# Optimization experiments

Hardware: AMD Instinct MI355X
Metric: run time of the kernel (lower is better)

The kernel has to match this reference:

```python
import jax, jax.numpy as jnp
import numpy as np

B, S, D = 4, 2048, 1024
H = 16
HD = D // H  # head dim = 64


def setup_inputs() -> dict:
    key = jax.random.key(0)
    ks = jax.random.split(key, 9)
    sc = 1.0 / np.sqrt(D)
    return {
        "x": jax.random.normal(ks[0], (B, S, D), jnp.float32),
        "Wq_w": jax.random.normal(ks[1], (D, D), jnp.float32) * sc,
        "Wq_b": jax.random.normal(ks[2], (D,), jnp.float32) * 0.01,
        "Wk_w": jax.random.normal(ks[3], (D, D), jnp.float32) * sc,
        "Wk_b": jax.random.normal(ks[4], (D,), jnp.float32) * 0.01,
        "Wv_w": jax.random.normal(ks[5], (D, D), jnp.float32) * sc,
        "Wv_b": jax.random.normal(ks[6], (D,), jnp.float32) * 0.01,
        "Wo_w": jax.random.normal(ks[7], (D, D), jnp.float32) * sc,
        "Wo_b": jax.random.normal(ks[8], (D,), jnp.float32) * 0.01,
    }


def reference(x, Wq_w, Wq_b, Wk_w, Wk_b, Wv_w, Wv_b, Wo_w, Wo_b):
    b, s, _ = x.shape
    # QKV projections (weights stored [in, out])
    q = x @ Wq_w + Wq_b
    k = x @ Wk_w + Wk_b
    v = x @ Wv_w + Wv_b
    # [b, s, D] -> [b, H, s, hd]
    q = q.reshape(b, s, H, HD).transpose(0, 2, 1, 3)
    k = k.reshape(b, s, H, HD).transpose(0, 2, 1, 3)
    v = v.reshape(b, s, H, HD).transpose(0, 2, 1, 3)
    # naive attention: full [b, H, s, s] scores, scale by head_dim**0.5
    scores = jnp.einsum("bhqd,bhkd->bhqk", q, k) / jnp.sqrt(jnp.float32(HD))
    # faithful to torch: tril(scores)==0 -> -inf (causal mask via tril of values)
    filt = jnp.tril(scores)
    scores = jnp.where(filt == 0, jnp.float32(-jnp.inf), scores)
    probs = jax.nn.softmax(scores, axis=-1)
    attn = jnp.einsum("bhqk,bhkd->bhqd", probs, v)
    # [b, H, s, hd] -> [b, s, D]
    attn = attn.transpose(0, 2, 1, 3).reshape(b, s, D)
    return attn @ Wo_w + Wo_b
```

## Files before the change

### kernel.cpp

```cpp
#include <hip/hip_runtime.h>
#include <hip/hip_bf16.h>


#define B_  4
#define S_  2048
#define D_  1024
#define H_  16
#define HD_ 64
#define M_  (B_*S_)
#define NT_ (S_/64)

typedef unsigned short u16;
typedef __attribute__((ext_vector_type(8))) short bf16x8;
typedef __attribute__((ext_vector_type(4))) float f32x4;
typedef __attribute__((ext_vector_type(8))) unsigned short ush8;
typedef __attribute__((ext_vector_type(4))) unsigned short ush4;

static __device__ __forceinline__ u16 f2b(float f) {
    unsigned int u = __float_as_uint(f);
    return (u16)((u + 0x7fffu + ((u >> 16) & 1u)) >> 16);
}

static __device__ __forceinline__ int cvt_pk_bf16(float a, float b) {
    int r;
    asm("v_cvt_pk_bf16_f32 %0, %1, %2" : "=v"(r) : "v"(a), "v"(b));
    return r;
}

#define EXP2(x) exp2f(x)

#define GLOAD_LDS16(g, l)                                                      \
    __builtin_amdgcn_global_load_lds(                                          \
        (const __attribute__((address_space(1))) void*)(g),                    \
        (__attribute__((address_space(3))) void*)(l), 16, 0, 0)

#define QSCALE 0.18033688f

__global__ __launch_bounds__(256)
void cast_f32_bf16(const float* __restrict__ in, u16* __restrict__ out, int n8)
{
    int i = blockIdx.x * blockDim.x + threadIdx.x;
    const int stride = gridDim.x * blockDim.x;
    for (; i < n8; i += stride) {
        const float4 a = ((const float4*)in)[i*2+0];
        const float4 b = ((const float4*)in)[i*2+1];
        ush8 o;
        o[0]=f2b(a.x); o[1]=f2b(a.y); o[2]=f2b(a.z); o[3]=f2b(a.w);
        o[4]=f2b(b.x); o[5]=f2b(b.y); o[6]=f2b(b.z); o[7]=f2b(b.w);
        ((ush8*)out)[i] = o;
    }
}

__global__ __launch_bounds__(256)
void transpose_cast(const float* __restrict__ W, u16* __restrict__ Wt)
{
    __shared__ u16 T[64*72];
    const int tid = threadIdx.x;
    const int k0 = blockIdx.x * 64, n0 = blockIdx.y * 64;
    #pragma unroll
    for (int it = 0; it < 4; ++it) {
        const int li = tid + it*256;
        const int kk = li >> 4;
        const int nc = (li & 15) * 4;
        const float4 w4 = *(const float4*)&W[(size_t)(k0+kk)*D_ + n0 + nc];
        T[(nc+0)*72 + kk] = f2b(w4.x);
        T[(nc+1)*72 + kk] = f2b(w4.y);
        T[(nc+2)*72 + kk] = f2b(w4.z);
        T[(nc+3)*72 + kk] = f2b(w4.w);
    }
    __syncthreads();
    #pragma unroll
    for (int it = 0; it < 2; ++it) {
        const int li = tid + it*256;
        const int nr = li >> 3;
        const int kc = (li & 7) * 8;
        const ush8 v = *(const ush8*)&T[nr*72 + kc];
        *(ush8*)&Wt[(size_t)(n0+nr)*D_ + k0 + kc] = v;
    }
}

__device__ __forceinline__ void gemm256_loop(
    const u16* __restrict__ Ag, size_t arow0,
    const u16* __restrict__ Bg, size_t brow0,
    u16* __restrict__ sh, f32x4 (&acc)[8][4])
{
    const int tid  = threadIdx.x;
    const int lane = tid & 63;
    const int wave = tid >> 6;
    const int wr = wave >> 2, wc = wave & 3;
    const int cl = lane & 15, g = lane >> 4;
    const int sw = cl & 7;
    u16* const Ab = sh;
    u16* const Bb = sh + 32768;

    const int srow   = lane >> 3;
    const int schunk = (lane & 7) ^ srow;

    auto stage_half = [&](const u16* gbase, size_t row0, int k0, u16* lbase) {
        #pragma unroll
        for (int i = 0; i < 2; ++i) {
            const int seg = wave*2 + i;
            const u16* src = gbase + (row0 + seg*8 + srow) * (size_t)D_
                                   + k0 + schunk*8;
            u16* dst = lbase + seg*512;
            GLOAD_LDS16(src, dst);
        }
    };

    stage_half(Ag, arow0,       0, Ab);
    stage_half(Ag, arow0 + 128, 0, Ab + 8192);
    stage_half(Bg, brow0,       0, Bb);
    stage_half(Bg, brow0 + 128, 0, Bb + 8192);
    __syncthreads();

    for (int t = 0; t < 16; ++t) {
        u16* const Ac = Ab + (t & 1) * 16384;
        u16* const Bc = Bb + (t & 1) * 16384;
        u16* const An = Ab + ((t + 1) & 1) * 16384;
        u16* const Bn = Bb + ((t + 1) & 1) * 16384;
        const int  kn   = (t + 1) * 64;
        const bool more = (t < 15);

        bf16x8 bfr[4][2];
        #pragma unroll
        for (int nf = 0; nf < 4; ++nf)
            #pragma unroll
            for (int ks = 0; ks < 2; ++ks)
                bfr[nf][ks] = *(const bf16x8*)
                    &Bc[(wc*64 + nf*16 + cl)*64 + (((ks*4 + g) ^ sw) * 8)];

        #pragma unroll
        for (int p = 0; p < 4; ++p) {
            bf16x8 af[2][2];
            #pragma unroll
            for (int e = 0; e < 2; ++e)
                #pragma unroll
                for (int ks = 0; ks < 2; ++ks)
                    af[e][ks] = *(const bf16x8*)
                        &Ac[(wr*128 + (p*2 + e)*16 + cl)*64
                            + (((ks*4 + g) ^ sw) * 8)];

            if (p == 0 && more) {
                stage_half(Ag, arow0,       kn, An);
                stage_half(Ag, arow0 + 128, kn, An + 8192);
            } else if (p == 1 && more) {
                stage_half(Bg, brow0,       kn, Bn);
                stage_half(Bg, brow0 + 128, kn, Bn + 8192);
            }

            __builtin_amdgcn_sched_barrier(0);
            __builtin_amdgcn_s_barrier();
            __builtin_amdgcn_sched_barrier(0);

            __builtin_amdgcn_s_setprio(1);
            #pragma unroll
            for (int e = 0; e < 2; ++e)
                #pragma unroll
                for (int ks = 0; ks < 2; ++ks)
                    #pragma unroll
                    for (int nf = 0; nf < 4; ++nf)
                        acc[p*2 + e][nf] = __builtin_amdgcn_mfma_f32_16x16x32_bf16(
                            af[e][ks], bfr[nf][ks], acc[p*2 + e][nf], 0, 0, 0);
            __builtin_amdgcn_s_setprio(0);

            if (p == 3) {
                asm volatile("s_waitcnt vmcnt(0)" ::: "memory");
            }
            __builtin_amdgcn_sched_barrier(0);
            __builtin_amdgcn_s_barrier();
            __builtin_amdgcn_sched_barrier(0);
        }
    }
    __syncthreads();
}

__global__ __launch_bounds__(512, 2)
void gemm_qkv256(const u16* __restrict__ A,
                 const u16* __restrict__ wq, const u16* __restrict__ wk,
                 const u16* __restrict__ wv,
                 const float* __restrict__ bq, const float* __restrict__ bk,
                 const float* __restrict__ bv,
                 u16* __restrict__ oq, u16* __restrict__ ok,
                 u16* __restrict__ ovt)
{
    __shared__ u16 sh[67584];

    const int tid  = threadIdx.x;
    const int lane = tid & 63;
    const int wave = tid >> 6;
    const int wr = wave >> 2, wc = wave & 3;
    const int cl = lane & 15, g = lane >> 4;
    const size_t bm = (size_t)blockIdx.x * 256;
    const int by   = blockIdx.y;
    const int sel  = by >> 2;
    const int bn2  = (by & 3) * 256;
    const u16* Bt = sel == 0 ? wq : sel == 1 ? wk : wv;
    const float* bias = sel == 0 ? bq : sel == 1 ? bk : bv;

    f32x4 acc[8][4];
    const f32x4 z4 = {0.f, 0.f, 0.f, 0.f};
    #pragma unroll
    for (int i = 0; i < 8; ++i)
        #pragma unroll
        for (int j = 0; j < 4; ++j) acc[i][j] = z4;

    gemm256_loop(A, bm, Bt, (size_t)bn2, sh, acc);

    if (sel == 2) {
        const int b  = (int)(bm >> 11);
        const int s0 = (int)(bm & (S_ - 1));
        #pragma unroll
        for (int nf = 0; nf < 4; ++nf) {
            const float bvv = bias[bn2 + wc*64 + nf*16 + cl];
            #pragma unroll
            for (int mf = 0; mf < 8; ++mf) {
                ush4 o4;
                #pragma unroll
                for (int r = 0; r < 4; ++r) o4[r] = f2b(acc[mf][nf][r] + bvv);
                *(ush4*)&sh[wc*16896 + (nf*16 + cl)*264 + wr*128 + mf*16 + g*4] = o4;
            }
        }
        __syncthreads();
        const int head = wave >> 1, shalf = wave & 1;
        const int hh = (bn2 >> 6) + head;
        #pragma unroll
        for (int it = 0; it < 16; ++it) {
            const int lin = it*64 + lane;
            const int d = lin >> 4, sc = lin & 15;
            const ush8 vv = *(const ush8*)&sh[head*16896 + d*264 + shalf*128 + sc*8];
            *(ush8*)&ovt[((size_t)((b*H_ + hh)*HD_ + d))*S_ + s0 + shalf*128 + sc*8] = vv;
        }
    } else {
        const float osc = sel == 0 ? QSCALE : 1.0f;
        u16* o = sel == 0 ? oq : ok;
        #pragma unroll
        for (int nf = 0; nf < 4; ++nf) {
            const int col = bn2 + wc*64 + nf*16 + cl;
            const float bvv = bias[col];
            const int h = col >> 6, d = col & (HD_ - 1);
            #pragma unroll
            for (int mf = 0; mf < 8; ++mf) {
                #pragma unroll
                for (int r = 0; r < 4; ++r) {
                    const size_t row = bm + wr*128 + mf*16 + g*4 + r;
                    const int bb = (int)(row >> 11), s = (int)(row & (S_ - 1));
                    o[((size_t)(bb*H_ + h)*S_ + s)*HD_ + d] =
                        f2b((acc[mf][nf][r] + bvv) * osc);
                }
            }
        }
    }
}

__global__ __launch_bounds__(512, 2)
void gemm_oproj256(const u16* __restrict__ A, const u16* __restrict__ Bt,
                   const float* __restrict__ bias, float* __restrict__ out)
{
    __shared__ u16 sh[65536];

    const int tid  = threadIdx.x;
    const int lane = tid & 63;
    const int wave = tid >> 6;
    const int wr = wave >> 2, wc = wave & 3;
    const int cl = lane & 15, g = lane >> 4;
    const size_t bm = (size_t)blockIdx.x * 256;
    const size_t bn = (size_t)blockIdx.y * 256;

    f32x4 acc[8][4];
    const f32x4 z4 = {0.f, 0.f, 0.f, 0.f};
    #pragma unroll
    for (int i = 0; i < 8; ++i)
        #pragma unroll
        for (int j = 0; j < 4; ++j) acc[i][j] = z4;

    gemm256_loop(A, bm, Bt, bn, sh, acc);

    #pragma unroll
    for (int nf = 0; nf < 4; ++nf) {
        const int col = (int)bn + wc*64 + nf*16 + cl;
        const float bvv = bias[col];
        #pragma unroll
        for (int mf = 0; mf < 8; ++mf) {
            #pragma unroll
            for (int r = 0; r < 4; ++r) {
                const size_t row = bm + wr*128 + mf*16 + g*4 + r;
                out[row*D_ + col] = acc[mf][nf][r] + bvv;
            }
        }
    }
}

__global__ __launch_bounds__(256, 4)
void attn_bf16(const u16* __restrict__ Q, const u16* __restrict__ K,
               const u16* __restrict__ Vt, u16* __restrict__ out)
{
    __shared__ u16 Ks[2][64*64];
    __shared__ u16 Vs[2][64*64];

    const int tid  = threadIdx.x;
    const int lane = tid & 63;
    const int wave = tid >> 6;
    const int cl = lane & 15;
    const int g  = lane >> 4;
    const int swz = cl & 7;
    const int pair = blockIdx.x, h = blockIdx.y, b = blockIdx.z;
    const size_t base  = ((size_t)(b*H_ + h)) * S_ * HD_;
    const size_t vbase = ((size_t)(b*H_ + h)) * HD_ * S_;

    int qt = pair;
    const int n0 = pair + 1;

    const int r0 = tid >> 3;
    const int c0 = tid & 7;

    bf16x8 qf[2];
    #pragma unroll
    for (int ks = 0; ks < 2; ++ks)
        qf[ks] = *(const bf16x8*)&Q[base +
            (size_t)(qt*64 + wave*16 + cl)*HD_ + ks*32 + g*8];

    ush8 kreg[2], vreg[2];
    #pragma unroll
    for (int p = 0; p < 2; ++p) {
        kreg[p] = *(const ush8*)&K [base  + (size_t)(r0 + p*32)*HD_ + c0*8];
        vreg[p] = *(const ush8*)&Vt[vbase + (size_t)(r0 + p*32)*S_  + c0*8];
    }

    const f32x4 z4 = {0.f, 0.f, 0.f, 0.f};
    f32x4 oac[4];
    float m_i = -3.0e38f, l_i = 0.f;
    #pragma unroll
    for (int nf = 0; nf < 4; ++nf) oac[nf] = z4;

    int cur = 0;
    for (int t = 0; t < NT_ + 1; ++t) {
        const int kt = (t >= n0) ? t - n0 : t;

        if (t == n0) {
            const float inv = 1.f / l_i;
            const int srow = qt*64 + wave*16 + cl;
            #pragma unroll
            for (int nf = 0; nf < 4; ++nf) {
                ush4 o4;
                #pragma unroll
                for (int r = 0; r < 4; ++r) o4[r] = f2b(oac[nf][r] * inv);
                *(ush4*)&out[(size_t)(b*S_ + srow)*D_ + h*HD_ + nf*16 + g*4] = o4;
            }
            qt = NT_ - 1 - pair;
            #pragma unroll
            for (int ks = 0; ks < 2; ++ks)
                qf[ks] = *(const bf16x8*)&Q[base +
                    (size_t)(qt*64 + wave*16 + cl)*HD_ + ks*32 + g*8];
            m_i = -3.0e38f; l_i = 0.f;
            #pragma unroll
            for (int nf = 0; nf < 4; ++nf) oac[nf] = z4;
        }

        #pragma unroll
        for (int p = 0; p < 2; ++p) {
            const int row = r0 + p*32;
            const int slot = (c0 ^ (row & 7)) * 8;
            *(ush8*)&Ks[cur][row*64 + slot] = kreg[p];
            *(ush8*)&Vs[cur][row*64 + slot] = vreg[p];
        }
        __syncthreads();

        if (t + 1 < NT_ + 1) {
            const int nkt = (t + 1 >= n0) ? t + 1 - n0 : t + 1;
            #pragma unroll
            for (int p = 0; p < 2; ++p) {
                kreg[p] = *(const ush8*)&K [base  +
                    (size_t)(nkt*64 + r0 + p*32)*HD_ + c0*8];
                vreg[p] = *(const ush8*)&Vt[vbase +
                    (size_t)(r0 + p*32)*S_ + nkt*64 + c0*8];
            }
        }

        f32x4 sac[4];
        #pragma unroll
        for (int nf = 0; nf < 4; ++nf) sac[nf] = z4;
        __builtin_amdgcn_s_setprio(1);
        #pragma unroll
        for (int ks = 0; ks < 2; ++ks) {
            const int slot = ((ks*4 + g) ^ swz) * 8;
            #pragma unroll
            for (int nf = 0; nf < 4; ++nf) {
                const bf16x8 kf =
                    *(const bf16x8*)&Ks[cur][(nf*16 + cl)*64 + slot];
                sac[nf] = __builtin_amdgcn_mfma_f32_16x16x32_bf16(
                    kf, qf[ks], sac[nf], 0, 0, 0);
            }
        }
        __builtin_amdgcn_s_setprio(0);

        if (kt == qt) {
            const int qloc = wave*16 + cl;
            #pragma unroll
            for (int nf = 0; nf < 4; ++nf)
                #pragma unroll
                for (int r = 0; r < 4; ++r)
                    if (nf*16 + g*4 + r > qloc) sac[nf][r] = -3.0e38f;
        }

        float mx = -3.0e38f;
        #pragma unroll
        for (int nf = 0; nf < 4; ++nf)
            #pragma unroll
            for (int r = 0; r < 4; ++r) mx = fmaxf(mx, sac[nf][r]);
        mx = fmaxf(mx, __shfl_xor(mx, 16));
        mx = fmaxf(mx, __shfl_xor(mx, 32));
        const float mnew = fmaxf(m_i, mx);
        const float es = EXP2(m_i - mnew);
        float ls = 0.f;
        #pragma unroll
        for (int nf = 0; nf < 4; ++nf) {
            float s0 = EXP2(sac[nf][0] - mnew);
            float s1 = EXP2(sac[nf][1] - mnew);
            float s2 = EXP2(sac[nf][2] - mnew);
            float s3 = EXP2(sac[nf][3] - mnew);
            sac[nf][0] = s0; sac[nf][1] = s1; sac[nf][2] = s2; sac[nf][3] = s3;
            ls += (s0 + s1) + (s2 + s3);
        }
        ls += __shfl_xor(ls, 16);
        ls += __shfl_xor(ls, 32);
        m_i = mnew;
        l_i = l_i * es + ls;
        #pragma unroll
        for (int nf = 0; nf < 4; ++nf)
            #pragma unroll
            for (int r = 0; r < 4; ++r) oac[nf][r] *= es;

        int X[4], Y[4];
        #pragma unroll
        for (int nf = 0; nf < 4; ++nf) {
            X[nf] = cvt_pk_bf16(sac[nf][0], sac[nf][1]);
            Y[nf] = cvt_pk_bf16(sac[nf][2], sac[nf][3]);
        }

        const int sA = cl + ((g & 1) << 5);
        const bool hi = (g >> 1) != 0;
        __builtin_amdgcn_s_setprio(1);
        #pragma unroll
        for (int ks = 0; ks < 2; ++ks) {
            const int x0 = __shfl(X[2*ks],   sA);
            const int x1 = __shfl(X[2*ks+1], sA);
            const int y0 = __shfl(Y[2*ks],   sA);
            const int y1 = __shfl(Y[2*ks+1], sA);
            const int x2 = __shfl(X[2*ks],   sA + 16);
            const int x3 = __shfl(X[2*ks+1], sA + 16);
            const int y2 = __shfl(Y[2*ks],   sA + 16);
            const int y3 = __shfl(Y[2*ks+1], sA + 16);
            int4 w;
            w.x = hi ? x1 : x0;
            w.y = hi ? y1 : y0;
            w.z = hi ? x3 : x2;
            w.w = hi ? y3 : y2;
            const bf16x8 pb = __builtin_bit_cast(bf16x8, w);
            const int slot = ((ks*4 + g) ^ swz) * 8;
            #pragma unroll
            for (int nfd = 0; nfd < 4; ++nfd) {
                const bf16x8 vf =
                    *(const bf16x8*)&Vs[cur][(nfd*16 + cl)*64 + slot];
                oac[nfd] = __builtin_amdgcn_mfma_f32_16x16x32_bf16(
                    vf, pb, oac[nfd], 0, 0, 0);
            }
        }
        __builtin_amdgcn_s_setprio(0);
        cur ^= 1;
    }

    {
        const float inv = 1.f / l_i;
        const int srow = qt*64 + wave*16 + cl;
        #pragma unroll
        for (int nf = 0; nf < 4; ++nf) {
            ush4 o4;
            #pragma unroll
            for (int r = 0; r < 4; ++r) o4[r] = f2b(oac[nf][r] * inv);
            *(ush4*)&out[(size_t)(b*S_ + srow)*D_ + h*HD_ + nf*16 + g*4] = o4;
        }
    }
}

extern "C" void kernel_launch(void* const* d_in, const int* in_sizes, int n_in,
                              void* d_out, int out_size, void* d_ws, size_t ws_size,
                              hipStream_t stream)
{
    const float* x    = (const float*)d_in[0];
    const float* Wq_w = (const float*)d_in[1];
    const float* Wq_b = (const float*)d_in[2];
    const float* Wk_w = (const float*)d_in[3];
    const float* Wk_b = (const float*)d_in[4];
    const float* Wv_w = (const float*)d_in[5];
    const float* Wv_b = (const float*)d_in[6];
    const float* Wo_w = (const float*)d_in[7];
    const float* Wo_b = (const float*)d_in[8];
    float* out = (float*)d_out;

    u16* xb    = (u16*)d_ws;
    u16* wqt   = xb  + (size_t)M_*D_;
    u16* wkt   = wqt + (size_t)D_*D_;
    u16* wvt   = wkt + (size_t)D_*D_;
    u16* wot   = wvt + (size_t)D_*D_;
    u16* q     = wot + (size_t)D_*D_;
    u16* k     = q   + (size_t)M_*D_;
    u16* vt    = k   + (size_t)M_*D_;
    u16* attnb = vt  + (size_t)M_*D_;

    cast_f32_bf16<<<2048, 256, 0, stream>>>(x, xb, M_*D_/8);
    transpose_cast<<<dim3(16,16), 256, 0, stream>>>(Wq_w, wqt);
    transpose_cast<<<dim3(16,16), 256, 0, stream>>>(Wk_w, wkt);
    transpose_cast<<<dim3(16,16), 256, 0, stream>>>(Wv_w, wvt);
    transpose_cast<<<dim3(16,16), 256, 0, stream>>>(Wo_w, wot);

    gemm_qkv256<<<dim3(M_/256, 12), 512, 0, stream>>>(
        xb, wqt, wkt, wvt, Wq_b, Wk_b, Wv_b, q, k, vt);

    attn_bf16<<<dim3(NT_/2, H_, B_), 256, 0, stream>>>(q, k, vt, attnb);

    gemm_oproj256<<<dim3(M_/256, D_/256), 512, 0, stream>>>(attnb, wot, Wo_b, out);
}
```

Baseline: 293.7 us.

## Shrink GEMM tiles to 128, widen attention to 128-row query blocks, merge transposes

The QKV and output projection GEMMs move from 256x256 tiles with 512 threads to 128x128 tiles with 256 threads and a simpler double-buffered loop that has one barrier per k-step. Attention now runs 512-thread blocks that each handle 128 query rows, sharing every K/V tile across 8 waves, and pairs q-tiles for causal load balance. The four weight transpose launches are fused into one grid. The smaller GEMM tiles give more blocks but less data reuse per block, and the larger attention blocks reuse K/V loads more but add masking work on the diagonal tiles.

```diff
diff --git a/kernel.cpp b/kernel.cpp
--- a/kernel.cpp
+++ b/kernel.cpp
@@ -8,7 +8,7 @@
 #define H_  16
 #define HD_ 64
 #define M_  (B_*S_)
-#define NT_ (S_/64)
+#define NKV_ 32
 
 typedef unsigned short u16;
 typedef __attribute__((ext_vector_type(8))) short bf16x8;
@@ -52,9 +52,15 @@
 }
 
 __global__ __launch_bounds__(256)
-void transpose_cast(const float* __restrict__ W, u16* __restrict__ Wt)
+void transpose_cast4(const float* __restrict__ W0, const float* __restrict__ W1,
+                     const float* __restrict__ W2, const float* __restrict__ W3,
+                     u16* __restrict__ T0, u16* __restrict__ T1,
+                     u16* __restrict__ T2, u16* __restrict__ T3)
 {
     __shared__ u16 T[64*72];
+    const int z = blockIdx.z;
+    const float* W = z == 0 ? W0 : z == 1 ? W1 : z == 2 ? W2 : W3;
+    u16* Wt = z == 0 ? T0 : z == 1 ? T1 : z == 2 ? T2 : T3;
     const int tid = threadIdx.x;
     const int k0 = blockIdx.x * 64, n0 = blockIdx.y * 64;
     #pragma unroll
@@ -79,103 +85,74 @@
     }
 }
 
-__device__ __forceinline__ void gemm256_loop(
+__device__ __forceinline__ void gemm128_core(
     const u16* __restrict__ Ag, size_t arow0,
     const u16* __restrict__ Bg, size_t brow0,
-    u16* __restrict__ sh, f32x4 (&acc)[8][4])
+    u16* __restrict__ sh, f32x4 (&acc)[4][4])
 {
     const int tid  = threadIdx.x;
     const int lane = tid & 63;
     const int wave = tid >> 6;
-    const int wr = wave >> 2, wc = wave & 3;
+    const int wr = wave >> 1, wc = wave & 1;
     const int cl = lane & 15, g = lane >> 4;
     const int sw = cl & 7;
-    u16* const Ab = sh;
-    u16* const Bb = sh + 32768;
-
     const int srow   = lane >> 3;
     const int schunk = (lane & 7) ^ srow;
-
-    auto stage_half = [&](const u16* gbase, size_t row0, int k0, u16* lbase) {
-        #pragma unroll
-        for (int i = 0; i < 2; ++i) {
-            const int seg = wave*2 + i;
-            const u16* src = gbase + (row0 + seg*8 + srow) * (size_t)D_
-                                   + k0 + schunk*8;
-            u16* dst = lbase + seg*512;
-            GLOAD_LDS16(src, dst);
+    u16* const Ab = sh;
+    u16* const Bb = sh + 16384;
+
+    auto stage = [&](int k0, u16* la, u16* lb) {
+        #pragma unroll
+        for (int i = 0; i < 4; ++i) {
+            const int seg = wave*4 + i;
+            GLOAD_LDS16(Ag + (arow0 + seg*8 + srow)*(size_t)D_ + k0 + schunk*8,
+                        la + seg*512);
+            GLOAD_LDS16(Bg + (brow0 + seg*8 + srow)*(size_t)D_ + k0 + schunk*8,
+                        lb + seg*512);
         }
     };
 
-    stage_half(Ag, arow0,       0, Ab);
-    stage_half(Ag, arow0 + 128, 0, Ab + 8192);
-    stage_half(Bg, brow0,       0, Bb);
-    stage_half(Bg, brow0 + 128, 0, Bb + 8192);
+    stage(0, Ab, Bb);
     __syncthreads();
 
     for (int t = 0; t < 16; ++t) {
-        u16* const Ac = Ab + (t & 1) * 16384;
-        u16* const Bc = Bb + (t & 1) * 16384;
-        u16* const An = Ab + ((t + 1) & 1) * 16384;
-        u16* const Bn = Bb + ((t + 1) & 1) * 16384;
-        const int  kn   = (t + 1) * 64;
-        const bool more = (t < 15);
-
-        bf16x8 bfr[4][2];
+        u16* const Ac = Ab + (t & 1) * 8192;
+        u16* const Bc = Bb + (t & 1) * 8192;
+
+        bf16x8 af[4][2], bf[4][2];
+        #pragma unroll
+        for (int mf = 0; mf < 4; ++mf)
+            #pragma unroll
+            for (int ks = 0; ks < 2; ++ks)
+                af[mf][ks] = *(const bf16x8*)
+                    &Ac[(wr*64 + mf*16 + cl)*64 + (((ks*4 + g) ^ sw) * 8)];
         #pragma unroll
         for (int nf = 0; nf < 4; ++nf)
             #pragma unroll
             for (int ks = 0; ks < 2; ++ks)
-                bfr[nf][ks] = *(const bf16x8*)
+                bf[nf][ks] = *(const bf16x8*)
                     &Bc[(wc*64 + nf*16 + cl)*64 + (((ks*4 + g) ^ sw) * 8)];
 
-        #pragma unroll
-        for (int p = 0; p < 4; ++p) {
-            bf16x8 af[2][2];
-            #pragma unroll
-            for (int e = 0; e < 2; ++e)
+        if (t < 15)
+            stage((t + 1) * 64, Ab + ((t + 1) & 1) * 8192,
+                                Bb + ((t + 1) & 1) * 8192);
+
+        __builtin_amdgcn_s_setprio(1);
+        #pragma unroll
+        for (int ks = 0; ks < 2; ++ks)
+            #pragma unroll
+            for (int mf = 0; mf < 4; ++mf)
                 #pragma unroll
-                for (int ks = 0; ks < 2; ++ks)
-                    af[e][ks] = *(const bf16x8*)
-                        &Ac[(wr*128 + (p*2 + e)*16 + cl)*64
-                            + (((ks*4 + g) ^ sw) * 8)];
-
-            if (p == 0 && more) {
-                stage_half(Ag, arow0,       kn, An);
-                stage_half(Ag, arow0 + 128, kn, An + 8192);
-            } else if (p == 1 && more) {
-                stage_half(Bg, brow0,       kn, Bn);
-                stage_half(Bg, brow0 + 128, kn, Bn + 8192);
-            }
-
-            __builtin_amdgcn_sched_barrier(0);
-            __builtin_amdgcn_s_barrier();
-            __builtin_amdgcn_sched_barrier(0);
-
-            __builtin_amdgcn_s_setprio(1);
-            #pragma unroll
-            for (int e = 0; e < 2; ++e)
-                #pragma unroll
-                for (int ks = 0; ks < 2; ++ks)
-                    #pragma unroll
-                    for (int nf = 0; nf < 4; ++nf)
-                        acc[p*2 + e][nf] = __builtin_amdgcn_mfma_f32_16x16x32_bf16(
-                            af[e][ks], bfr[nf][ks], acc[p*2 + e][nf], 0, 0, 0);
-            __builtin_amdgcn_s_setprio(0);
-
-            if (p == 3) {
-                asm volatile("s_waitcnt vmcnt(0)" ::: "memory");
-            }
-            __builtin_amdgcn_sched_barrier(0);
-            __builtin_amdgcn_s_barrier();
-            __builtin_amdgcn_sched_barrier(0);
-        }
-    }
-    __syncthreads();
-}
-
-__global__ __launch_bounds__(512, 2)
-void gemm_qkv256(const u16* __restrict__ A,
+                for (int nf = 0; nf < 4; ++nf)
+                    acc[mf][nf] = __builtin_amdgcn_mfma_f32_16x16x32_bf16(
+                        af[mf][ks], bf[nf][ks], acc[mf][nf], 0, 0, 0);
+        __builtin_amdgcn_s_setprio(0);
+        __syncthreads();
+    }
+}
+
+__global__ __launch_bounds__(256, 2)
+void gemm_qkv128(const u16* __restrict__ A,
                  const u16* __restrict__ wq, const u16* __restrict__ wk,
                  const u16* __restrict__ wv,
                  const float* __restrict__ bq, const float* __restrict__ bk,
@@ -183,66 +160,66 @@
                  u16* __restrict__ oq, u16* __restrict__ ok,
                  u16* __restrict__ ovt)
 {
-    __shared__ u16 sh[67584];
-
+    __shared__ u16 sh[32768];
     const int tid  = threadIdx.x;
     const int lane = tid & 63;
     const int wave = tid >> 6;
-    const int wr = wave >> 2, wc = wave & 3;
+    const int wr = wave >> 1, wc = wave & 1;
     const int cl = lane & 15, g = lane >> 4;
-    const size_t bm = (size_t)blockIdx.x * 256;
-    const int by   = blockIdx.y;
-    const int sel  = by >> 2;
-    const int bn2  = (by & 3) * 256;
+    const size_t bm = (size_t)blockIdx.x * 128;
+    const int by  = blockIdx.y;
+    const int sel = by >> 3;
+    const int bn  = (by & 7) * 128;
     const u16* Bt = sel == 0 ? wq : sel == 1 ? wk : wv;
     const float* bias = sel == 0 ? bq : sel == 1 ? bk : bv;
 
-    f32x4 acc[8][4];
+    f32x4 acc[4][4];
     const f32x4 z4 = {0.f, 0.f, 0.f, 0.f};
     #pragma unroll
-    for (int i = 0; i < 8; ++i)
+    for (int i = 0; i < 4; ++i)
         #pragma unroll
         for (int j = 0; j < 4; ++j) acc[i][j] = z4;
 
-    gemm256_loop(A, bm, Bt, (size_t)bn2, sh, acc);
+    gemm128_core(A, bm, Bt, (size_t)bn, sh, acc);
 
     if (sel == 2) {
         const int b  = (int)(bm >> 11);
         const int s0 = (int)(bm & (S_ - 1));
         #pragma unroll
         for (int nf = 0; nf < 4; ++nf) {
-            const float bvv = bias[bn2 + wc*64 + nf*16 + cl];
-            #pragma unroll
-            for (int mf = 0; mf < 8; ++mf) {
+            const int col = wc*64 + nf*16 + cl;
+            const float bvv = bias[bn + col];
+            #pragma unroll
+            for (int mf = 0; mf < 4; ++mf) {
                 ush4 o4;
                 #pragma unroll
                 for (int r = 0; r < 4; ++r) o4[r] = f2b(acc[mf][nf][r] + bvv);
-                *(ush4*)&sh[wc*16896 + (nf*16 + cl)*264 + wr*128 + mf*16 + g*4] = o4;
+                *(ush4*)&sh[col*136 + wr*64 + mf*16 + g*4] = o4;
             }
         }
         __syncthreads();
-        const int head = wave >> 1, shalf = wave & 1;
-        const int hh = (bn2 >> 6) + head;
-        #pragma unroll
-        for (int it = 0; it < 16; ++it) {
-            const int lin = it*64 + lane;
-            const int d = lin >> 4, sc = lin & 15;
-            const ush8 vv = *(const ush8*)&sh[head*16896 + d*264 + shalf*128 + sc*8];
-            *(ush8*)&ovt[((size_t)((b*H_ + hh)*HD_ + d))*S_ + s0 + shalf*128 + sc*8] = vv;
+        #pragma unroll
+        for (int it = 0; it < 8; ++it) {
+            const int lin = it*256 + tid;
+            const int d2 = lin >> 4, sc = lin & 15;
+            const int hh = (bn >> 6) + (d2 >> 6);
+            const int d  = d2 & 63;
+            const ush8 vv = *(const ush8*)&sh[d2*136 + sc*8];
+            *(ush8*)&ovt[((size_t)((b*H_ + hh)*HD_ + d))*S_ + s0 + sc*8] = vv;
         }
     } else {
         const float osc = sel == 0 ? QSCALE : 1.0f;
         u16* o = sel == 0 ? oq : ok;
         #pragma unroll
         for (int nf = 0; nf < 4; ++nf) {
-            const int col = bn2 + wc*64 + nf*16 + cl;
+            const int col = bn + wc*64 + nf*16 + cl;
             const float bvv = bias[col];
             const int h = col >> 6, d = col & (HD_ - 1);
             #pragma unroll
-            for (int mf = 0; mf < 8; ++mf) {
+            for (int mf = 0; mf < 4; ++mf) {
                 #pragma unroll
                 for (int r = 0; r < 4; ++r) {
-                    const size_t row = bm + wr*128 + mf*16 + g*4 + r;
+                    const size_t row = bm + wr*64 + mf*16 + g*4 + r;
                     const int bb = (int)(row >> 11), s = (int)(row & (S_ - 1));
                     o[((size_t)(bb*H_ + h)*S_ + s)*HD_ + d] =
                         f2b((acc[mf][nf][r] + bvv) * osc);
@@ -252,45 +229,44 @@
     }
 }
 
-__global__ __launch_bounds__(512, 2)
-void gemm_oproj256(const u16* __restrict__ A, const u16* __restrict__ Bt,
+__global__ __launch_bounds__(256, 2)
+void gemm_oproj128(const u16* __restrict__ A, const u16* __restrict__ Bt,
                    const float* __restrict__ bias, float* __restrict__ out)
 {
-    __shared__ u16 sh[65536];
-
+    __shared__ u16 sh[32768];
     const int tid  = threadIdx.x;
     const int lane = tid & 63;
     const int wave = tid >> 6;
-    const int wr = wave >> 2, wc = wave & 3;
+    const int wr = wave >> 1, wc = wave & 1;
     const int cl = lane & 15, g = lane >> 4;
-    const size_t bm = (size_t)blockIdx.x * 256;
-    const size_t bn = (size_t)blockIdx.y * 256;
-
-    f32x4 acc[8][4];
+    const size_t bm = (size_t)blockIdx.x * 128;
+    const size_t bn = (size_t)blockIdx.y * 128;
+
+    f32x4 acc[4][4];
     const f32x4 z4 = {0.f, 0.f, 0.f, 0.f};
     #pragma unroll
-    for (int i = 0; i < 8; ++i)
+    for (int i = 0; i < 4; ++i)
         #pragma unroll
         for (int j = 0; j < 4; ++j) acc[i][j] = z4;
 
-    gemm256_loop(A, bm, Bt, bn, sh, acc);
+    gemm128_core(A, bm, Bt, bn, sh, acc);
 
     #pragma unroll
     for (int nf = 0; nf < 4; ++nf) {
         const int col = (int)bn + wc*64 + nf*16 + cl;
         const float bvv = bias[col];
         #pragma unroll
-        for (int mf = 0; mf < 8; ++mf) {
+        for (int mf = 0; mf < 4; ++mf) {
             #pragma unroll
             for (int r = 0; r < 4; ++r) {
-                const size_t row = bm + wr*128 + mf*16 + g*4 + r;
+                const size_t row = bm + wr*64 + mf*16 + g*4 + r;
                 out[row*D_ + col] = acc[mf][nf][r] + bvv;
             }
         }
     }
 }
 
-__global__ __launch_bounds__(256, 4)
+__global__ __launch_bounds__(512, 2)
 void attn_bf16(const u16* __restrict__ Q, const u16* __restrict__ K,
                const u16* __restrict__ Vt, u16* __restrict__ out)
 {
@@ -307,8 +283,8 @@
     const size_t base  = ((size_t)(b*H_ + h)) * S_ * HD_;
     const size_t vbase = ((size_t)(b*H_ + h)) * HD_ * S_;
 
-    int qt = pair;
-    const int n0 = pair + 1;
+    int qt2 = pair;
+    const int n0 = 2*pair + 2;
 
     const int r0 = tid >> 3;
     const int c0 = tid & 7;
@@ -317,14 +293,11 @@
     #pragma unroll
     for (int ks = 0; ks < 2; ++ks)
         qf[ks] = *(const bf16x8*)&Q[base +
-            (size_t)(qt*64 + wave*16 + cl)*HD_ + ks*32 + g*8];
-
-    ush8 kreg[2], vreg[2];
-    #pragma unroll
-    for (int p = 0; p < 2; ++p) {
-        kreg[p] = *(const ush8*)&K [base  + (size_t)(r0 + p*32)*HD_ + c0*8];
-        vreg[p] = *(const ush8*)&Vt[vbase + (size_t)(r0 + p*32)*S_  + c0*8];
-    }
+            (size_t)(qt2*128 + wave*16 + cl)*HD_ + ks*32 + g*8];
+
+    ush8 kreg, vreg;
+    kreg = *(const ush8*)&K [base  + (size_t)r0*HD_ + c0*8];
+    vreg = *(const ush8*)&Vt[vbase + (size_t)r0*S_  + c0*8];
 
     const f32x4 z4 = {0.f, 0.f, 0.f, 0.f};
     f32x4 oac[4];
@@ -333,12 +306,12 @@
     for (int nf = 0; nf < 4; ++nf) oac[nf] = z4;
 
     int cur = 0;
-    for (int t = 0; t < NT_ + 1; ++t) {
+    for (int t = 0; t < 34; ++t) {
         const int kt = (t >= n0) ? t - n0 : t;
 
         if (t == n0) {
             const float inv = 1.f / l_i;
-            const int srow = qt*64 + wave*16 + cl;
+            const int srow = qt2*128 + wave*16 + cl;
             #pragma unroll
             for (int nf = 0; nf < 4; ++nf) {
                 ush4 o4;
@@ -346,34 +319,27 @@
                 for (int r = 0; r < 4; ++r) o4[r] = f2b(oac[nf][r] * inv);
                 *(ush4*)&out[(size_t)(b*S_ + srow)*D_ + h*HD_ + nf*16 + g*4] = o4;
             }
-            qt = NT_ - 1 - pair;
+            qt2 = 15 - pair;
             #pragma unroll
             for (int ks = 0; ks < 2; ++ks)
                 qf[ks] = *(const bf16x8*)&Q[base +
-                    (size_t)(qt*64 + wave*16 + cl)*HD_ + ks*32 + g*8];
+                    (size_t)(qt2*128 + wave*16 + cl)*HD_ + ks*32 + g*8];
             m_i = -3.0e38f; l_i = 0.f;
             #pragma unroll
             for (int nf = 0; nf < 4; ++nf) oac[nf] = z4;
         }
 
-        #pragma unroll
-        for (int p = 0; p < 2; ++p) {
-            const int row = r0 + p*32;
-            const int slot = (c0 ^ (row & 7)) * 8;
-            *(ush8*)&Ks[cur][row*64 + slot] = kreg[p];
-            *(ush8*)&Vs[cur][row*64 + slot] = vreg[p];
+        {
+            const int slot = (c0 ^ (r0 & 7)) * 8;
+            *(ush8*)&Ks[cur][r0*64 + slot] = kreg;
+            *(ush8*)&Vs[cur][r0*64 + slot] = vreg;
         }
         __syncthreads();
 
-        if (t + 1 < NT_ + 1) {
+        if (t + 1 < 34) {
             const int nkt = (t + 1 >= n0) ? t + 1 - n0 : t + 1;
-            #pragma unroll
-            for (int p = 0; p < 2; ++p) {
-                kreg[p] = *(const ush8*)&K [base  +
-                    (size_t)(nkt*64 + r0 + p*32)*HD_ + c0*8];
-                vreg[p] = *(const ush8*)&Vt[vbase +
-                    (size_t)(r0 + p*32)*S_ + nkt*64 + c0*8];
-            }
+            kreg = *(const ush8*)&K [base  + (size_t)(nkt*64 + r0)*HD_ + c0*8];
+            vreg = *(const ush8*)&Vt[vbase + (size_t)r0*S_ + nkt*64 + c0*8];
         }
 
         f32x4 sac[4];
@@ -393,13 +359,14 @@
         }
         __builtin_amdgcn_s_setprio(0);
 
-        if (kt == qt) {
+        const int dkt = kt - 2*qt2;
+        if (dkt >= 0) {
             const int qloc = wave*16 + cl;
             #pragma unroll
             for (int nf = 0; nf < 4; ++nf)
                 #pragma unroll
                 for (int r = 0; r < 4; ++r)
-                    if (nf*16 + g*4 + r > qloc) sac[nf][r] = -3.0e38f;
+                    if (dkt*64 + nf*16 + g*4 + r > qloc) sac[nf][r] = -3.0e38f;
         }
 
         float mx = -3.0e38f;
@@ -471,7 +438,7 @@
 
     {
         const float inv = 1.f / l_i;
-        const int srow = qt*64 + wave*16 + cl;
+        const int srow = qt2*128 + wave*16 + cl;
         #pragma unroll
         for (int nf = 0; nf < 4; ++nf) {
             ush4 o4;
@@ -508,15 +475,13 @@
     u16* attnb = vt  + (size_t)M_*D_;
 
     cast_f32_bf16<<<2048, 256, 0, stream>>>(x, xb, M_*D_/8);
-    transpose_cast<<<dim3(16,16), 256, 0, stream>>>(Wq_w, wqt);
-    transpose_cast<<<dim3(16,16), 256, 0, stream>>>(Wk_w, wkt);
-    transpose_cast<<<dim3(16,16), 256, 0, stream>>>(Wv_w, wvt);
-    transpose_cast<<<dim3(16,16), 256, 0, stream>>>(Wo_w, wot);
-
-    gemm_qkv256<<<dim3(M_/256, 12), 512, 0, stream>>>(
+    transpose_cast4<<<dim3(16,16,4), 256, 0, stream>>>(
+        Wq_w, Wk_w, Wv_w, Wo_w, wqt, wkt, wvt, wot);
+
+    gemm_qkv128<<<dim3(M_/128, 24), 256, 0, stream>>>(
         xb, wqt, wkt, wvt, Wq_b, Wk_b, Wv_b, q, k, vt);
 
-    attn_bf16<<<dim3(NT_/2, H_, B_), 256, 0, stream>>>(q, k, vt, attnb);
-
-    gemm_oproj256<<<dim3(M_/256, D_/256), 512, 0, stream>>>(attnb, wot, Wo_b, out);
-}
+    attn_bf16<<<dim3(8, H_, B_), 512, 0, stream>>>(q, k, vt, attnb);
+
+    gemm_oproj128<<<dim3(M_/128, D_/128), 256, 0, stream>>>(attnb, wot, Wo_b, out);
+}
```

Result: faster. 272.8 us (-7.1%).
